# Optimization experiments

Hardware: AMD Instinct MI355X
Metric: run time of the kernel (lower is better)

Reference implementation:

```python
import jax, jax.numpy as jnp
import numpy as np

# dims: batch, q-heads, kv-heads, seq, head_dim, block size, window (kv blocks per q block)
B, H, KVH, S, D = 2, 16, 4, 4096, 64
BLK, W = 64, 8
G = H // KVH          # heads per group = 4
NQ = S // BLK         # 64 query blocks
L = W * BLK           # flattened kv window per q block = 512


def setup_inputs() -> dict:
    key = jax.random.key(0)
    k0, k1, k2, k3 = jax.random.split(key, 4)
    q = jax.random.normal(k0, (B, H, S, D), jnp.float32)
    k = jax.random.normal(k1, (B, KVH, S, D), jnp.float32)
    v = jax.random.normal(k2, (B, KVH, S, D), jnp.float32)
    # standard alibi slopes 2^(-8i/H)
    alibi_slopes = jnp.asarray(2.0 ** (-8.0 * np.arange(1, H + 1) / H), jnp.float32)
    # contiguous segments via sorted random ids
    segment_ids = jnp.sort(jax.random.randint(k3, (B, S), 0, 8, jnp.int32), axis=-1)
    # causal sliding window: q block qb attends to kv blocks [qb-W+1, qb]; -1 = invalid
    qb = np.arange(NQ)[:, None]
    bi = qb - (W - 1) + np.arange(W)[None, :]
    block_indices = jnp.asarray(np.where(bi < 0, -1, bi), jnp.int32)  # [NQ, W]
    return {"q": q, "k": k, "v": v, "alibi_slopes": alibi_slopes,
            "segment_ids": segment_ids, "block_indices": block_indices}


def reference(q, k, v, alibi_slopes, segment_ids, block_indices):
    scale = jnp.float32(1.0 / np.sqrt(D))
    NEG = jnp.float32(-1e30)

    qg = q.reshape(B, KVH, G, NQ, BLK, D)          # GQA grouping
    kb = k.reshape(B, KVH, NQ, BLK, D)
    vb = v.reshape(B, KVH, NQ, BLK, D)

    safe = jnp.clip(block_indices, 0)               # [NQ, W]
    kg = kb[:, :, safe]                             # [B,KVH,NQ,W,BLK,D] gathered kv blocks
    vg = vb[:, :, safe]

    pos_m = (jnp.arange(NQ) * BLK)[:, None] + jnp.arange(BLK)             # [NQ,BM]
    pos_n = safe[:, :, None] * BLK + jnp.arange(BLK)[None, None, :]       # [NQ,W,BN]

    valid = (block_indices >= 0)[:, None, :, None]                        # [NQ,1,W,1]
    causal = pos_m[:, :, None, None] >= pos_n[:, None, :, :]              # [NQ,BM,W,BN]
    seg_q = segment_ids.reshape(B, NQ, BLK)
    seg_k = jnp.take(segment_ids, pos_n.reshape(-1), axis=1).reshape(B, NQ, W, BLK)
    same_seg = (seg_q[:, :, :, None, None] == seg_k[:, :, None, :, :]) & (seg_q[:, :, :, None, None] >= 0)
    mask = ((valid & causal)[None] & same_seg)                            # [B,NQ,BM,W,BN]
    maskb = mask.reshape(B, 1, 1, NQ, BLK, L)                             # broadcast over KVH,G

    scores = jnp.einsum('bkgqmd,bkqwnd->bkgqmwn', qg, kg) * scale         # [B,KVH,G,NQ,BM,W,BN]
    pos_diff = jnp.abs(pos_m[:, :, None, None] - pos_n[:, None, :, :]).astype(jnp.float32)
    scores = scores - alibi_slopes.reshape(KVH, G)[None, :, :, None, None, None, None] * pos_diff
    scores = scores.reshape(B, KVH, G, NQ, BLK, L)
    scores = jnp.where(maskb, scores, NEG)

    row_max = jnp.max(scores, axis=-1, keepdims=True)
    p = jnp.where(maskb, jnp.exp(scores - row_max), 0.0)
    l = jnp.sum(p, axis=-1, keepdims=True)                                # [B,KVH,G,NQ,BM,1]
    vf = vg.reshape(B, KVH, NQ, L, D)
    acc = jnp.einsum('bkgqml,bkqld->bkgqmd', p, vf)
    out = jnp.where(l > 0, acc / jnp.where(l > 0, l, 1.0), 0.0)           # zero rows with no valid kv
    return out.reshape(B, H, S, D)
```

## Files before the change

### kernel.cpp

```cpp
#include <hip/hip_runtime.h>
#include <hip/hip_bf16.h>

#define NKVH 4
#define SEQ 4096
#define BLK 64
#define NW 8
#define NQB 64
#define PP 72

typedef __attribute__((ext_vector_type(8))) short bf16x8;
typedef __attribute__((ext_vector_type(4))) float f32x4;

__device__ __forceinline__ unsigned pkbf(unsigned lo, unsigned hi) {
  return __builtin_amdgcn_perm(hi + 0x8000u, lo + 0x8000u, 0x07060302u);
}

__device__ __forceinline__ void gload16(const void* g, void* l) {
  __builtin_amdgcn_global_load_lds(
      (const __attribute__((address_space(1))) void*)g,
      (__attribute__((address_space(3))) void*)l, 16, 0, 0);
}

__global__ __launch_bounds__(256, 4)
void prep_kernel(const float* __restrict__ kp, const float* __restrict__ vp,
                 short* __restrict__ kw, short* __restrict__ vt)
{
  const int ki = blockIdx.x, kvh = blockIdx.y, b = blockIdx.z;
  const size_t base = (((size_t)(b*NKVH + kvh)*SEQ) + (size_t)ki*BLK)*64;
  __shared__ float vlds[64][65];
  const int t = threadIdx.x;
  #pragma unroll
  for (int it = 0; it < 2; ++it) {
    const int task = t + it*256;
    const int n = task >> 3, c8 = task & 7;
    const float* krow = kp + base + n*64 + c8*8;
    float4 a = *(const float4*)krow;
    float4 c = *(const float4*)(krow + 4);
    uint4 o;
    o.x = pkbf(__float_as_uint(a.x), __float_as_uint(a.y));
    o.y = pkbf(__float_as_uint(a.z), __float_as_uint(a.w));
    o.z = pkbf(__float_as_uint(c.x), __float_as_uint(c.y));
    o.w = pkbf(__float_as_uint(c.z), __float_as_uint(c.w));
    *(uint4*)(kw + base + n*64 + ((c8 ^ (n & 7)) * 8)) = o;
    const float* vrow = vp + base + n*64 + c8*8;
    float4 va = *(const float4*)vrow;
    float4 vc = *(const float4*)(vrow + 4);
    vlds[n][c8*8+0] = va.x; vlds[n][c8*8+1] = va.y;
    vlds[n][c8*8+2] = va.z; vlds[n][c8*8+3] = va.w;
    vlds[n][c8*8+4] = vc.x; vlds[n][c8*8+5] = vc.y;
    vlds[n][c8*8+6] = vc.z; vlds[n][c8*8+7] = vc.w;
  }
  __syncthreads();
  #pragma unroll
  for (int it = 0; it < 2; ++it) {
    const int task = t + it*256;
    const int d = task >> 3, cn = task & 7;
    float x0 = vlds[cn*8+0][d], x1 = vlds[cn*8+1][d];
    float x2 = vlds[cn*8+2][d], x3 = vlds[cn*8+3][d];
    float x4 = vlds[cn*8+4][d], x5 = vlds[cn*8+5][d];
    float x6 = vlds[cn*8+6][d], x7 = vlds[cn*8+7][d];
    uint4 o;
    o.x = pkbf(__float_as_uint(x0), __float_as_uint(x1));
    o.y = pkbf(__float_as_uint(x2), __float_as_uint(x3));
    o.z = pkbf(__float_as_uint(x4), __float_as_uint(x5));
    o.w = pkbf(__float_as_uint(x6), __float_as_uint(x7));
    *(uint4*)(vt + base + d*64 + ((cn ^ (d & 7)) * 8)) = o;
  }
}

__global__ __launch_bounds__(512, 2)
void sattn_kernel(const float* __restrict__ qp, const short* __restrict__ kw,
                  const short* __restrict__ vt, const float* __restrict__ alibi,
                  const int* __restrict__ seg, const int* __restrict__ bidx,
                  float* __restrict__ outp)
{
  const int bid = blockIdx.x + NQB*(blockIdx.y + NKVH*blockIdx.z);
  const int nl = (bid & 7)*64 + (bid >> 3);
  const int qb = nl & 63, kvh = (nl >> 6) & 3, b = nl >> 8;

  const int tid = threadIdx.x;
  const int wave = tid >> 6, lane = tid & 63;
  const int lr = lane & 15, lg = lane >> 4;
  const int wr = wave & 3, hp = wave >> 2;

  __shared__ short klds[2][BLK][64];
  __shared__ short vtlds[2][BLK][64];
  __shared__ short plds[8][16][PP];
  __shared__ int   seglds[NW][BLK];

  int kis[NW];
  #pragma unroll
  for (int i = 0; i < NW; ++i) kis[i] = bidx[qb*NW + i];

  const size_t headbase = ((size_t)(b*NKVH + kvh)*SEQ)*64;

  auto STAGE = [&](int buf, int wi) {
    const int ki = kis[wi] < 0 ? 0 : kis[wi];
    const size_t tb = headbase + (size_t)ki*BLK*64;
    gload16((const char*)(kw + tb) + tid*16, (char*)&klds[buf][0][0] + wave*1024);
    gload16((const char*)(vt + tb) + tid*16, (char*)&vtlds[buf][0][0] + wave*1024);
  };

  STAGE(0, 0);
  {
    const int wi = wave, j = lane;
    const int kiw = kis[wi];
    seglds[wi][j] = (kiw < 0) ? -1 : seg[b*SEQ + kiw*BLK + j];
  }

  const int m_glob = qb*BLK + wr*16 + lr;
  const int sq = seg[b*SEQ + m_glob];

  const float LOG2E = 1.4426950408889634f;
  float nslope[2];
  nslope[0] = -alibi[kvh*4 + hp*2 + 0] * LOG2E;
  nslope[1] = -alibi[kvh*4 + hp*2 + 1] * LOG2E;

  bf16x8 qf[2][2];
  {
    const float qs = 0.125f * LOG2E;
    #pragma unroll
    for (int hh = 0; hh < 2; ++hh) {
      const float* qrow = qp + ((((size_t)b*16 + kvh*4 + hp*2 + hh)*SEQ) + m_glob)*64;
      #pragma unroll
      for (int s = 0; s < 2; ++s) {
        float4 a = *(const float4*)(qrow + s*32 + lg*8);
        float4 c = *(const float4*)(qrow + s*32 + lg*8 + 4);
        union { unsigned u[4]; bf16x8 v; } cv;
        cv.u[0] = pkbf(__float_as_uint(a.x*qs), __float_as_uint(a.y*qs));
        cv.u[1] = pkbf(__float_as_uint(a.z*qs), __float_as_uint(a.w*qs));
        cv.u[2] = pkbf(__float_as_uint(c.x*qs), __float_as_uint(c.y*qs));
        cv.u[3] = pkbf(__float_as_uint(c.z*qs), __float_as_uint(c.w*qs));
        qf[hh][s] = cv.v;
      }
    }
  }

  float mrun[2] = {-1e30f, -1e30f}, lrun[2] = {0.f, 0.f};
  f32x4 oacc[2][4];
  #pragma unroll
  for (int hh = 0; hh < 2; ++hh)
    #pragma unroll
    for (int dt = 0; dt < 4; ++dt) { f32x4 z = {0.f,0.f,0.f,0.f}; oacc[hh][dt] = z; }

  __syncthreads();

  #pragma unroll
  for (int wi = 0; wi < NW; ++wi) {
    const int cur = wi & 1;
    if (wi + 1 < NW) STAGE(cur ^ 1, wi + 1);
    if (kis[wi] >= 0) {
      const int ki = kis[wi];
      int4 skv[4];
      #pragma unroll
      for (int f = 0; f < 4; ++f) skv[f] = *(const int4*)&seglds[wi][f*16 + lg*4];

      bf16x8 kf[2][4], vf[2][4];
      #pragma unroll
      for (int s = 0; s < 2; ++s)
        #pragma unroll
        for (int f = 0; f < 4; ++f) {
          const int cc = ((s*4 + lg) ^ (lr & 7)) * 8;
          kf[s][f] = *(const bf16x8*)&klds[cur][f*16 + lr][cc];
          vf[s][f] = *(const bf16x8*)&vtlds[cur][f*16 + lr][cc];
        }

      float pdm[4][4];
      #pragma unroll
      for (int f = 0; f < 4; ++f) {
        const int skr[4] = {skv[f].x, skv[f].y, skv[f].z, skv[f].w};
        #pragma unroll
        for (int r = 0; r < 4; ++r) {
          const int n_glob = ki*BLK + f*16 + lg*4 + r;
          const bool dead = (n_glob > m_glob) || (skr[r] != sq);
          pdm[f][r] = dead ? 3.0e34f : (float)(m_glob - n_glob);
        }
      }

      #pragma unroll
      for (int hh = 0; hh < 2; ++hh) {
        f32x4 sacc[4];
        #pragma unroll
        for (int f = 0; f < 4; ++f) { f32x4 z = {0.f,0.f,0.f,0.f}; sacc[f] = z; }
        #pragma unroll
        for (int s = 0; s < 2; ++s)
          #pragma unroll
          for (int f = 0; f < 4; ++f)
            sacc[f] = __builtin_amdgcn_mfma_f32_16x16x32_bf16(kf[s][f], qf[hh][s], sacc[f], 0, 0, 0);

        float mblk = -3.0e38f;
        #pragma unroll
        for (int f = 0; f < 4; ++f)
          #pragma unroll
          for (int r = 0; r < 4; ++r) {
            sacc[f][r] = fmaf(nslope[hh], pdm[f][r], sacc[f][r]);
            mblk = fmaxf(mblk, sacc[f][r]);
          }
        mblk = fmaxf(mblk, __shfl_xor(mblk, 16));
        mblk = fmaxf(mblk, __shfl_xor(mblk, 32));
        const float mnew = fmaxf(mrun[hh], mblk);
        const float corr = __builtin_amdgcn_exp2f(mrun[hh] - mnew);
        mrun[hh] = mnew;

        float psum = 0.f;
        #pragma unroll
        for (int f = 0; f < 4; ++f)
          #pragma unroll
          for (int rp = 0; rp < 2; ++rp) {
            float p0 = __builtin_amdgcn_exp2f(sacc[f][2*rp]   - mnew);
            float p1 = __builtin_amdgcn_exp2f(sacc[f][2*rp+1] - mnew);
            psum += p0 + p1;
            *(unsigned*)&plds[wave][lr][f*16 + lg*4 + 2*rp] =
                pkbf(__float_as_uint(p0), __float_as_uint(p1));
          }
        psum += __shfl_xor(psum, 16);
        psum += __shfl_xor(psum, 32);
        lrun[hh] = lrun[hh]*corr + psum;
        #pragma unroll
        for (int dt = 0; dt < 4; ++dt) oacc[hh][dt] *= corr;

        #pragma unroll
        for (int s = 0; s < 2; ++s) {
          bf16x8 pf = *(const bf16x8*)&plds[wave][lr][s*32 + lg*8];
          #pragma unroll
          for (int dt = 0; dt < 4; ++dt)
            oacc[hh][dt] = __builtin_amdgcn_mfma_f32_16x16x32_bf16(vf[s][dt], pf, oacc[hh][dt], 0, 0, 0);
        }
      }
    }
    __syncthreads();
  }

  #pragma unroll
  for (int hh = 0; hh < 2; ++hh) {
    const float inv = lrun[hh] > 0.f ? 1.f/lrun[hh] : 0.f;
    float* dst = outp + ((((size_t)b*16 + kvh*4 + hp*2 + hh)*SEQ) + m_glob)*64;
    #pragma unroll
    for (int dt = 0; dt < 4; ++dt) {
      float4 o;
      o.x = oacc[hh][dt][0]*inv; o.y = oacc[hh][dt][1]*inv;
      o.z = oacc[hh][dt][2]*inv; o.w = oacc[hh][dt][3]*inv;
      *(float4*)&dst[dt*16 + lg*4] = o;
    }
  }
}

extern "C" void kernel_launch(void* const* d_in, const int* in_sizes, int n_in,
                              void* d_out, int out_size, void* d_ws, size_t ws_size,
                              hipStream_t stream) {
  const float* q    = (const float*)d_in[0];
  const float* k    = (const float*)d_in[1];
  const float* v    = (const float*)d_in[2];
  const float* al   = (const float*)d_in[3];
  const int*   sg   = (const int*)d_in[4];
  const int*   bi   = (const int*)d_in[5];
  short* kws = (short*)d_ws;
  short* vtws = (short*)((char*)d_ws + (size_t)(1u<<22));
  dim3 pgrid(NQB, NKVH, 2);
  prep_kernel<<<pgrid, 256, 0, stream>>>(k, v, kws, vtws);
  dim3 grid(NQB, NKVH, 2);
  sattn_kernel<<<grid, 512, 0, stream>>>(q, kws, vtws, al, sg, bi, (float*)d_out);
}
```

Measured before the change: 54.11 us.

## Load K/V fragments directly from global memory, split head pairs across blocks

Removes the LDS double-buffered K/V staging and per-window-step barriers, so each wave reads its bf16 K and V fragments straight from global memory (relying on L1/L2 for reuse). The grid grows to 1024 blocks of 256 threads, with head-pair moved from the wave index to the block index and an XCD-aware block mapping that keeps a (batch, kv-head) on one XCD. Both heads' QK MFMAs now share one K fragment load. The cost is redundant global/L2 traffic, since two blocks now fetch the same K/V, and there is no explicit prefetch to hide load latency.

```diff
diff --git a/kernel.cpp b/kernel.cpp
--- a/kernel.cpp
+++ b/kernel.cpp
@@ -13,12 +13,6 @@
 
 __device__ __forceinline__ unsigned pkbf(unsigned lo, unsigned hi) {
   return __builtin_amdgcn_perm(hi + 0x8000u, lo + 0x8000u, 0x07060302u);
-}
-
-__device__ __forceinline__ void gload16(const void* g, void* l) {
-  __builtin_amdgcn_global_load_lds(
-      (const __attribute__((address_space(1))) void*)g,
-      (__attribute__((address_space(3))) void*)l, 16, 0, 0);
 }
 
 __global__ __launch_bounds__(256, 4)
@@ -68,47 +62,32 @@
   }
 }
 
-__global__ __launch_bounds__(512, 2)
+__global__ __launch_bounds__(256, 4)
 void sattn_kernel(const float* __restrict__ qp, const short* __restrict__ kw,
                   const short* __restrict__ vt, const float* __restrict__ alibi,
                   const int* __restrict__ seg, const int* __restrict__ bidx,
                   float* __restrict__ outp)
 {
-  const int bid = blockIdx.x + NQB*(blockIdx.y + NKVH*blockIdx.z);
-  const int nl = (bid & 7)*64 + (bid >> 3);
-  const int qb = nl & 63, kvh = (nl >> 6) & 3, b = nl >> 8;
+  const int raw = blockIdx.x;
+  const int xcd = raw & 7, li = raw >> 3;
+  const int b = xcd >> 2, kvh = xcd & 3;
+  const int qb = li & 63, hp = li >> 6;
 
   const int tid = threadIdx.x;
   const int wave = tid >> 6, lane = tid & 63;
   const int lr = lane & 15, lg = lane >> 4;
-  const int wr = wave & 3, hp = wave >> 2;
-
-  __shared__ short klds[2][BLK][64];
-  __shared__ short vtlds[2][BLK][64];
-  __shared__ short plds[8][16][PP];
-  __shared__ int   seglds[NW][BLK];
-
-  int kis[NW];
-  #pragma unroll
-  for (int i = 0; i < NW; ++i) kis[i] = bidx[qb*NW + i];
-
-  const size_t headbase = ((size_t)(b*NKVH + kvh)*SEQ)*64;
-
-  auto STAGE = [&](int buf, int wi) {
-    const int ki = kis[wi] < 0 ? 0 : kis[wi];
-    const size_t tb = headbase + (size_t)ki*BLK*64;
-    gload16((const char*)(kw + tb) + tid*16, (char*)&klds[buf][0][0] + wave*1024);
-    gload16((const char*)(vt + tb) + tid*16, (char*)&vtlds[buf][0][0] + wave*1024);
-  };
-
-  STAGE(0, 0);
-  {
-    const int wi = wave, j = lane;
-    const int kiw = kis[wi];
-    seglds[wi][j] = (kiw < 0) ? -1 : seg[b*SEQ + kiw*BLK + j];
-  }
-
-  const int m_glob = qb*BLK + wr*16 + lr;
+
+  __shared__ short plds[4][16][PP];
+  __shared__ int seglds[NW][BLK];
+
+  #pragma unroll
+  for (int t = 0; t < 2; ++t) {
+    const int wi = wave + t*4;
+    const int kiw = bidx[qb*NW + wi];
+    seglds[wi][lane] = (kiw < 0) ? -1 : seg[b*SEQ + kiw*BLK + lane];
+  }
+
+  const int m_glob = qb*BLK + wave*16 + lr;
   const int sq = seg[b*SEQ + m_glob];
 
   const float LOG2E = 1.4426950408889634f;
@@ -143,92 +122,93 @@
     #pragma unroll
     for (int dt = 0; dt < 4; ++dt) { f32x4 z = {0.f,0.f,0.f,0.f}; oacc[hh][dt] = z; }
 
+  const short* kbase = kw + ((size_t)(b*NKVH + kvh)*SEQ)*64;
+  const short* vbase = vt + ((size_t)(b*NKVH + kvh)*SEQ)*64;
+  const int cc = (lg ^ (lr & 7)) * 8;
+  const int cc1 = ((4 + lg) ^ (lr & 7)) * 8;
+
   __syncthreads();
 
-  #pragma unroll
   for (int wi = 0; wi < NW; ++wi) {
-    const int cur = wi & 1;
-    if (wi + 1 < NW) STAGE(cur ^ 1, wi + 1);
-    if (kis[wi] >= 0) {
-      const int ki = kis[wi];
-      int4 skv[4];
-      #pragma unroll
-      for (int f = 0; f < 4; ++f) skv[f] = *(const int4*)&seglds[wi][f*16 + lg*4];
-
-      bf16x8 kf[2][4], vf[2][4];
-      #pragma unroll
-      for (int s = 0; s < 2; ++s)
-        #pragma unroll
-        for (int f = 0; f < 4; ++f) {
-          const int cc = ((s*4 + lg) ^ (lr & 7)) * 8;
-          kf[s][f] = *(const bf16x8*)&klds[cur][f*16 + lr][cc];
-          vf[s][f] = *(const bf16x8*)&vtlds[cur][f*16 + lr][cc];
-        }
-
-      float pdm[4][4];
+    const int ki = bidx[qb*NW + wi];
+    if (ki < 0) continue;
+    const short* kt = kbase + (size_t)ki*(BLK*64);
+    const short* vtt = vbase + (size_t)ki*(BLK*64);
+
+    int4 skv[4];
+    #pragma unroll
+    for (int f = 0; f < 4; ++f) skv[f] = *(const int4*)&seglds[wi][f*16 + lg*4];
+
+    f32x4 sacc2[2][4];
+    #pragma unroll
+    for (int hh = 0; hh < 2; ++hh)
+      #pragma unroll
+      for (int f = 0; f < 4; ++f) { f32x4 z = {0.f,0.f,0.f,0.f}; sacc2[hh][f] = z; }
+    #pragma unroll
+    for (int s = 0; s < 2; ++s)
       #pragma unroll
       for (int f = 0; f < 4; ++f) {
-        const int skr[4] = {skv[f].x, skv[f].y, skv[f].z, skv[f].w};
+        bf16x8 kf = *(const bf16x8*)(kt + (f*16 + lr)*64 + (s ? cc1 : cc));
+        sacc2[0][f] = __builtin_amdgcn_mfma_f32_16x16x32_bf16(kf, qf[0][s], sacc2[0][f], 0, 0, 0);
+        sacc2[1][f] = __builtin_amdgcn_mfma_f32_16x16x32_bf16(kf, qf[1][s], sacc2[1][f], 0, 0, 0);
+      }
+
+    float pdm[4][4];
+    #pragma unroll
+    for (int f = 0; f < 4; ++f) {
+      const int skr[4] = {skv[f].x, skv[f].y, skv[f].z, skv[f].w};
+      #pragma unroll
+      for (int r = 0; r < 4; ++r) {
+        const int n_glob = ki*BLK + f*16 + lg*4 + r;
+        const bool dead = (n_glob > m_glob) || (skr[r] != sq);
+        pdm[f][r] = dead ? 3.0e34f : (float)(m_glob - n_glob);
+      }
+    }
+
+    #pragma unroll
+    for (int hh = 0; hh < 2; ++hh) {
+      float sv[4][4];
+      float mblk = -3.0e38f;
+      #pragma unroll
+      for (int f = 0; f < 4; ++f)
         #pragma unroll
         for (int r = 0; r < 4; ++r) {
-          const int n_glob = ki*BLK + f*16 + lg*4 + r;
-          const bool dead = (n_glob > m_glob) || (skr[r] != sq);
-          pdm[f][r] = dead ? 3.0e34f : (float)(m_glob - n_glob);
+          sv[f][r] = fmaf(nslope[hh], pdm[f][r], sacc2[hh][f][r]);
+          mblk = fmaxf(mblk, sv[f][r]);
         }
-      }
-
-      #pragma unroll
-      for (int hh = 0; hh < 2; ++hh) {
-        f32x4 sacc[4];
+      mblk = fmaxf(mblk, __shfl_xor(mblk, 16));
+      mblk = fmaxf(mblk, __shfl_xor(mblk, 32));
+      const float mnew = fmaxf(mrun[hh], mblk);
+      const float corr = __builtin_amdgcn_exp2f(mrun[hh] - mnew);
+      mrun[hh] = mnew;
+
+      float psum = 0.f;
+      #pragma unroll
+      for (int f = 0; f < 4; ++f)
         #pragma unroll
-        for (int f = 0; f < 4; ++f) { f32x4 z = {0.f,0.f,0.f,0.f}; sacc[f] = z; }
+        for (int rp = 0; rp < 2; ++rp) {
+          float p0 = __builtin_amdgcn_exp2f(sv[f][2*rp]   - mnew);
+          float p1 = __builtin_amdgcn_exp2f(sv[f][2*rp+1] - mnew);
+          psum += p0 + p1;
+          *(unsigned*)&plds[wave][lr][f*16 + lg*4 + 2*rp] =
+              pkbf(__float_as_uint(p0), __float_as_uint(p1));
+        }
+      psum += __shfl_xor(psum, 16);
+      psum += __shfl_xor(psum, 32);
+      lrun[hh] = lrun[hh]*corr + psum;
+      #pragma unroll
+      for (int dt = 0; dt < 4; ++dt) oacc[hh][dt] *= corr;
+
+      #pragma unroll
+      for (int s = 0; s < 2; ++s) {
+        bf16x8 pf = *(const bf16x8*)&plds[wave][lr][s*32 + lg*8];
         #pragma unroll
-        for (int s = 0; s < 2; ++s)
-          #pragma unroll
-          for (int f = 0; f < 4; ++f)
-            sacc[f] = __builtin_amdgcn_mfma_f32_16x16x32_bf16(kf[s][f], qf[hh][s], sacc[f], 0, 0, 0);
-
-        float mblk = -3.0e38f;
-        #pragma unroll
-        for (int f = 0; f < 4; ++f)
-          #pragma unroll
-          for (int r = 0; r < 4; ++r) {
-            sacc[f][r] = fmaf(nslope[hh], pdm[f][r], sacc[f][r]);
-            mblk = fmaxf(mblk, sacc[f][r]);
-          }
-        mblk = fmaxf(mblk, __shfl_xor(mblk, 16));
-        mblk = fmaxf(mblk, __shfl_xor(mblk, 32));
-        const float mnew = fmaxf(mrun[hh], mblk);
-        const float corr = __builtin_amdgcn_exp2f(mrun[hh] - mnew);
-        mrun[hh] = mnew;
-
-        float psum = 0.f;
-        #pragma unroll
-        for (int f = 0; f < 4; ++f)
-          #pragma unroll
-          for (int rp = 0; rp < 2; ++rp) {
-            float p0 = __builtin_amdgcn_exp2f(sacc[f][2*rp]   - mnew);
-            float p1 = __builtin_amdgcn_exp2f(sacc[f][2*rp+1] - mnew);
-            psum += p0 + p1;
-            *(unsigned*)&plds[wave][lr][f*16 + lg*4 + 2*rp] =
-                pkbf(__float_as_uint(p0), __float_as_uint(p1));
-          }
-        psum += __shfl_xor(psum, 16);
-        psum += __shfl_xor(psum, 32);
-        lrun[hh] = lrun[hh]*corr + psum;
-        #pragma unroll
-        for (int dt = 0; dt < 4; ++dt) oacc[hh][dt] *= corr;
-
-        #pragma unroll
-        for (int s = 0; s < 2; ++s) {
-          bf16x8 pf = *(const bf16x8*)&plds[wave][lr][s*32 + lg*8];
-          #pragma unroll
-          for (int dt = 0; dt < 4; ++dt)
-            oacc[hh][dt] = __builtin_amdgcn_mfma_f32_16x16x32_bf16(vf[s][dt], pf, oacc[hh][dt], 0, 0, 0);
+        for (int dt = 0; dt < 4; ++dt) {
+          bf16x8 vf = *(const bf16x8*)(vtt + (dt*16 + lr)*64 + (s ? cc1 : cc));
+          oacc[hh][dt] = __builtin_amdgcn_mfma_f32_16x16x32_bf16(vf, pf, oacc[hh][dt], 0, 0, 0);
         }
       }
     }
-    __syncthreads();
   }
 
   #pragma unroll
@@ -258,6 +238,5 @@
   short* vtws = (short*)((char*)d_ws + (size_t)(1u<<22));
   dim3 pgrid(NQB, NKVH, 2);
   prep_kernel<<<pgrid, 256, 0, stream>>>(k, v, kws, vtws);
-  dim3 grid(NQB, NKVH, 2);
-  sattn_kernel<<<grid, 512, 0, stream>>>(q, kws, vtws, al, sg, bi, (float*)d_out);
-}
+  sattn_kernel<<<dim3(1024), 256, 0, stream>>>(q, kws, vtws, al, sg, bi, (float*)d_out);
+}
```

Measured after the change: 87.72 us. +62.1%, slower.
